# Optimization experiments

Measured on AMD Instinct MI355X. Metric: run time of the kernel, lower is better.

## Reference

```python
import jax, jax.numpy as jnp
import numpy as np
import math

S = 8192  # sequence length
D = 16    # model dim (8-dim one-hot embedding concatenated with its negation)


def _params():
    emb = np.eye(3, 8, dtype=np.float32)
    # ---- FirstLayer ----
    l1_in_w = np.zeros((48, 16), np.float32); l1_in_w[32, 0] = 1; l1_in_w[33, 1] = 1
    l1_in_b = np.zeros(48, np.float32)
    l1_out_w = np.zeros((16, 16), np.float32)
    l1_out_w[3, 0] = 1; l1_out_w[4, 1] = 1; l1_out_w[11, 0] = -1; l1_out_w[12, 1] = -1
    l1_out_b = np.zeros(16, np.float32)
    l1_w1 = np.zeros((16, 16), np.float32)
    l1_w1[5, 3] = 1; l1_w1[5, 4] = -1; l1_w1[6, 3] = -1; l1_w1[6, 4] = 1
    l1_b1 = np.zeros(16, np.float32)
    l1_w2 = np.zeros((16, 16), np.float32)
    l1_w2[5, 5] = 1; l1_w2[6, 6] = 1; l1_w2[7, 5] = 1; l1_w2[7, 6] = 1
    l1_w2[13, 5] = -1; l1_w2[14, 6] = -1; l1_w2[15, 5] = -1; l1_w2[15, 6] = -1
    l1_b2 = np.zeros(16, np.float32)
    # ---- SecondLayer ----
    l2_in_w = np.zeros((48, 16), np.float32)
    l2_in_b = np.zeros(48, np.float32)
    l2_out_w = np.zeros((16, 16), np.float32)
    l2_out_b = np.zeros(16, np.float32)
    l2_w1 = np.zeros((16, 16), np.float32)
    l2_w1[:8, :8] = np.eye(8); l2_w1[8:, :8] = -np.eye(8)
    l2_b1 = np.zeros(16, np.float32)
    A = np.zeros((16, 16), np.float32)
    A[:8, :8] = -np.eye(8); A[:8, 8:] = np.eye(8)
    A[8:, :8] = np.eye(8);  A[8:, 8:] = -np.eye(8)
    B = np.zeros((16, 16), np.float32)
    B[0, 7] = -1; B[0, 15] = 1; B[1, 7] = 1; B[1, 15] = -1
    l2_w2 = A + B
    l2_b2 = np.array([-1e-8] * 8 + [1e-8] * 8, np.float32)
    # ---- Output layer ----
    eta = 1e-5
    c = -(1.0 / math.sqrt(16.0 / 2.0)) * math.log(2.0 ** eta - 1.0)
    ow = np.zeros((1, 16), np.float32); ow[0, 0] = c
    ob = np.zeros(1, np.float32)
    names = ['emb', 'l1_in_w', 'l1_in_b', 'l1_out_w', 'l1_out_b', 'l1_w1', 'l1_b1', 'l1_w2', 'l1_b2',
             'l2_in_w', 'l2_in_b', 'l2_out_w', 'l2_out_b', 'l2_w1', 'l2_b1', 'l2_w2', 'l2_b2', 'ow', 'ob']
    vals = [emb, l1_in_w, l1_in_b, l1_out_w, l1_out_b, l1_w1, l1_b1, l1_w2, l1_b2,
            l2_in_w, l2_in_b, l2_out_w, l2_out_b, l2_w1, l2_b1, l2_w2, l2_b2, ow, ob]
    return {n: jnp.asarray(v) for n, v in zip(names, vals)}


def setup_inputs() -> dict:
    key = jax.random.key(0)
    w = jax.random.randint(key, (S,), 0, 3)
    inp = {'w': w}
    inp.update(_params())
    return inp


def _layernorm(x):
    # hand-rolled layernorm: (x - mean) / sqrt(E[x^2] - mean^2), no eps, no affine
    mean = jnp.mean(x, axis=-1, keepdims=True)
    var = jnp.mean(x * x, axis=-1, keepdims=True) - mean * mean
    return (x - mean) / jnp.sqrt(var)


def _layer(src, in_w, in_b, out_w, out_b, w1, b1, w2, b2):
    # src: [S, 16]; single-head MHA, dropout=0, relu activation
    qw, kw, vw = jnp.split(in_w, 3, axis=0)
    qb, kb, vb = jnp.split(in_b, 3)
    q = src @ qw.T + qb
    k = src @ kw.T + kb
    v = src @ vw.T + vb
    attn = jax.nn.softmax((q @ k.T) / math.sqrt(float(D)), axis=-1)  # [S, S]
    a = (attn @ v) @ out_w.T + out_b
    h = _layernorm(src + a)
    ff = jax.nn.relu(h @ w1.T + b1) @ w2.T + b2
    return _layernorm(h + ff)


def reference(w, emb, l1_in_w, l1_in_b, l1_out_w, l1_out_b, l1_w1, l1_b1, l1_w2, l1_b2,
              l2_in_w, l2_in_b, l2_out_w, l2_out_b, l2_w1, l2_b1, l2_w2, l2_b2, ow, ob):
    x = emb[w]                                    # [S, 8]
    src = jnp.concatenate([x, -x], axis=-1)       # [S, 16]
    src = _layer(src, l1_in_w, l1_in_b, l1_out_w, l1_out_b, l1_w1, l1_b1, l1_w2, l1_b2)
    src = _layer(src, l2_in_w, l2_in_b, l2_out_w, l2_out_b, l2_w1, l2_b1, l2_w2, l2_b2)
    return src[0] @ ow.T + ob                     # [1]
```

## Files before the change

kernel.cpp:

```cpp
#include <hip/hip_runtime.h>


#define NT 256

struct LayerRegs {
    float4 vw[4], ow[4], w1[4], w2[4];
    float vb, ob_, b1, b2;
};

__device__ __forceinline__ float gsum16(float v) {
    v += __shfl_xor(v, 1, 16);
    v += __shfl_xor(v, 2, 16);
    v += __shfl_xor(v, 4, 16);
    v += __shfl_xor(v, 8, 16);
    return v;
}

__device__ __forceinline__ float lnp(float x) {
    float s  = gsum16(x);
    float s2 = gsum16(x * x);
    float mean = s * 0.0625f;
    float msq  = s2 * 0.0625f;
    return (x - mean) * rsqrtf(msq - mean * mean);
}

__device__ __forceinline__ float matR(const float4* __restrict__ W, float b, float x) {
    float a0 = b, a1 = 0.f;
    #pragma unroll
    for (int kq = 0; kq < 4; ++kq) {
        float4 wv = W[kq];
        a0 += __shfl(x, 4 * kq + 0, 16) * wv.x;
        a1 += __shfl(x, 4 * kq + 1, 16) * wv.y;
        a0 += __shfl(x, 4 * kq + 2, 16) * wv.z;
        a1 += __shfl(x, 4 * kq + 3, 16) * wv.w;
    }
    return a0 + a1;
}

__device__ __forceinline__ float layer_lane(float src, float meansrc,
                                            const LayerRegs& L) {
    float vmean = matR(L.vw, L.vb,  meansrc);
    float a     = matR(L.ow, L.ob_, vmean);
    float h     = lnp(src + a);
    float r     = fmaxf(matR(L.w1, L.b1, h), 0.f);
    float y     = h + matR(L.w2, L.b2, r);
    return lnp(y);
}

#define LOADROW(dst, ptr, row) {                         \
    const float4* _p = (const float4*)(ptr) + (row) * 4; \
    dst[0] = _p[0]; dst[1] = _p[1];                      \
    dst[2] = _p[2]; dst[3] = _p[3]; }

__global__ void __launch_bounds__(NT)
model_kernel(const int* __restrict__ w, int S,
             const float* __restrict__ emb,
             const float* __restrict__ l1_in_w, const float* __restrict__ l1_in_b,
             const float* __restrict__ l1_out_w, const float* __restrict__ l1_out_b,
             const float* __restrict__ l1_w1, const float* __restrict__ l1_b1,
             const float* __restrict__ l1_w2, const float* __restrict__ l1_b2,
             const float* __restrict__ l2_in_w, const float* __restrict__ l2_in_b,
             const float* __restrict__ l2_out_w, const float* __restrict__ l2_out_b,
             const float* __restrict__ l2_w1, const float* __restrict__ l2_b1,
             const float* __restrict__ l2_w2, const float* __restrict__ l2_b2,
             const float* __restrict__ ow, const float* __restrict__ ob,
             float* __restrict__ out)
{
    __shared__ int cnt[2];
    const int tid = threadIdx.x;
    const int j   = tid & 15;
    const int jb  = j & 7;
    const bool w0wave = (tid < 64);
    if (tid < 2) cnt[tid] = 0;

    LayerRegs R1, R2;
    float e0 = 0.f, e1 = 0.f, e2 = 0.f, owj = 0.f, ob0 = 0.f;
    int t0 = 0;
    if (w0wave) {
        t0 = w[0];
        LOADROW(R1.vw, l1_in_w, 32 + j);
        LOADROW(R1.ow, l1_out_w, j);
        LOADROW(R1.w1, l1_w1, j);
        LOADROW(R1.w2, l1_w2, j);
        LOADROW(R2.vw, l2_in_w, 32 + j);
        LOADROW(R2.ow, l2_out_w, j);
        LOADROW(R2.w1, l2_w1, j);
        LOADROW(R2.w2, l2_w2, j);
        R1.vb = l1_in_b[32 + j]; R1.ob_ = l1_out_b[j];
        R1.b1 = l1_b1[j];        R1.b2  = l1_b2[j];
        R2.vb = l2_in_b[32 + j]; R2.ob_ = l2_out_b[j];
        R2.b1 = l2_b1[j];        R2.b2  = l2_b2[j];
        e0 = emb[jb]; e1 = emb[8 + jb]; e2 = emb[16 + jb];
        owj = ow[j];  ob0 = ob[0];
    }
    const float invS = 1.f / (float)S;

    int c0 = 0, c1 = 0;
    if (S == NT * 32) {
        const int4* w4 = (const int4*)w;
        int4 t[8];
        #pragma unroll
        for (int u = 0; u < 8; ++u) t[u] = w4[tid + u * NT];
        #pragma unroll
        for (int u = 0; u < 8; ++u) {
            c0 += (t[u].x == 0) + (t[u].y == 0) + (t[u].z == 0) + (t[u].w == 0);
            c1 += (t[u].x == 1) + (t[u].y == 1) + (t[u].z == 1) + (t[u].w == 1);
        }
    } else {
        for (int i = tid; i < S; i += NT) {
            int t = w[i];
            c0 += (t == 0); c1 += (t == 1);
        }
    }
    #pragma unroll
    for (int off = 32; off; off >>= 1) {
        c0 += __shfl_down(c0, off);
        c1 += __shfl_down(c1, off);
    }
    __syncthreads();
    if ((tid & 63) == 0) {
        atomicAdd(&cnt[0], c0);
        atomicAdd(&cnt[1], c1);
    }
    __syncthreads();
    if (!w0wave) return;

    const float p0 = cnt[0] * invS;
    const float p1 = cnt[1] * invS;
    const float p2 = 1.f - p0 - p1;
    const float sgn = (j < 8) ? 1.f : -1.f;

    const float meansrc = sgn * (p0 * e0 + p1 * e1 + p2 * e2);

    const float r0 = layer_lane(sgn * e0, meansrc, R1);
    const float r1 = layer_lane(sgn * e1, meansrc, R1);
    const float r2 = layer_lane(sgn * e2, meansrc, R1);

    const float meansrc1 = p0 * r0 + p1 * r1 + p2 * r2;
    const float src2 = (t0 == 0) ? r0 : (t0 == 1 ? r1 : r2);
    const float fin = layer_lane(src2, meansrc1, R2);

    const float dot = gsum16(fin * owj);
    if (tid == 0) out[0] = dot + ob0;
}

extern "C" void kernel_launch(void* const* d_in, const int* in_sizes, int n_in,
                              void* d_out, int out_size, void* d_ws, size_t ws_size,
                              hipStream_t stream) {
    const int*   w        = (const int*)  d_in[0];
    const int    S        = in_sizes[0];
    const float* emb      = (const float*)d_in[1];
    const float* l1_in_w  = (const float*)d_in[2];
    const float* l1_in_b  = (const float*)d_in[3];
    const float* l1_out_w = (const float*)d_in[4];
    const float* l1_out_b = (const float*)d_in[5];
    const float* l1_w1    = (const float*)d_in[6];
    const float* l1_b1    = (const float*)d_in[7];
    const float* l1_w2    = (const float*)d_in[8];
    const float* l1_b2    = (const float*)d_in[9];
    const float* l2_in_w  = (const float*)d_in[10];
    const float* l2_in_b  = (const float*)d_in[11];
    const float* l2_out_w = (const float*)d_in[12];
    const float* l2_out_b = (const float*)d_in[13];
    const float* l2_w1    = (const float*)d_in[14];
    const float* l2_b1    = (const float*)d_in[15];
    const float* l2_w2    = (const float*)d_in[16];
    const float* l2_b2    = (const float*)d_in[17];
    const float* ow       = (const float*)d_in[18];
    const float* ob       = (const float*)d_in[19];
    float* out = (float*)d_out;

    model_kernel<<<1, NT, 0, stream>>>(w, S, emb,
        l1_in_w, l1_in_b, l1_out_w, l1_out_b, l1_w1, l1_b1, l1_w2, l1_b2,
        l2_in_w, l2_in_b, l2_out_w, l2_out_b, l2_w1, l2_b1, l2_w2, l2_b2,
        ow, ob, out);
}
```

Baseline: 9.930 us.

## Overlap token counting with layer-1 precompute and use ds_swizzle broadcasts

Wave 0 no longer counts tokens. It precomputes the attention output per embedding linearly (u and cvec) while waves 1-3 count tokens with packed 16-bit counters and write per-wave partials to shared memory, removing the atomics and one barrier. The three per-token layer-1 evaluations run in parallel across the four 16-lane groups instead of serially, with cross-lane shuffles gathering results. The 16-lane shuffles become ds_swizzle with immediate patterns. Packing counts into 16 bits limits each count to 65535, and moving the attention output projection through linearity reorders floating-point sums.

```diff
diff --git a/kernel.cpp b/kernel.cpp
--- a/kernel.cpp
+++ b/kernel.cpp
@@ -3,16 +3,15 @@
 
 #define NT 256
 
-struct LayerRegs {
-    float4 vw[4], ow[4], w1[4], w2[4];
-    float vb, ob_, b1, b2;
-};
+template<int K> __device__ __forceinline__ float bc16(float v) {
+    return __int_as_float(__builtin_amdgcn_ds_swizzle(__float_as_int(v), 0x10 | (K << 5)));
+}
+template<int M> __device__ __forceinline__ float xr16(float v) {
+    return __int_as_float(__builtin_amdgcn_ds_swizzle(__float_as_int(v), 0x1f | (M << 10)));
+}
 
 __device__ __forceinline__ float gsum16(float v) {
-    v += __shfl_xor(v, 1, 16);
-    v += __shfl_xor(v, 2, 16);
-    v += __shfl_xor(v, 4, 16);
-    v += __shfl_xor(v, 8, 16);
+    v += xr16<1>(v); v += xr16<2>(v); v += xr16<4>(v); v += xr16<8>(v);
     return v;
 }
 
@@ -24,27 +23,22 @@
     return (x - mean) * rsqrtf(msq - mean * mean);
 }
 
+struct LayerRegs {
+    float4 vw[4], ow[4], w1[4], w2[4];
+    float vb, ob_, b1, b2;
+};
+
 __device__ __forceinline__ float matR(const float4* __restrict__ W, float b, float x) {
     float a0 = b, a1 = 0.f;
-    #pragma unroll
-    for (int kq = 0; kq < 4; ++kq) {
-        float4 wv = W[kq];
-        a0 += __shfl(x, 4 * kq + 0, 16) * wv.x;
-        a1 += __shfl(x, 4 * kq + 1, 16) * wv.y;
-        a0 += __shfl(x, 4 * kq + 2, 16) * wv.z;
-        a1 += __shfl(x, 4 * kq + 3, 16) * wv.w;
-    }
+    a0 += bc16<0 >(x) * W[0].x;  a1 += bc16<1 >(x) * W[0].y;
+    a0 += bc16<2 >(x) * W[0].z;  a1 += bc16<3 >(x) * W[0].w;
+    a0 += bc16<4 >(x) * W[1].x;  a1 += bc16<5 >(x) * W[1].y;
+    a0 += bc16<6 >(x) * W[1].z;  a1 += bc16<7 >(x) * W[1].w;
+    a0 += bc16<8 >(x) * W[2].x;  a1 += bc16<9 >(x) * W[2].y;
+    a0 += bc16<10>(x) * W[2].z;  a1 += bc16<11>(x) * W[2].w;
+    a0 += bc16<12>(x) * W[3].x;  a1 += bc16<13>(x) * W[3].y;
+    a0 += bc16<14>(x) * W[3].z;  a1 += bc16<15>(x) * W[3].w;
     return a0 + a1;
-}
-
-__device__ __forceinline__ float layer_lane(float src, float meansrc,
-                                            const LayerRegs& L) {
-    float vmean = matR(L.vw, L.vb,  meansrc);
-    float a     = matR(L.ow, L.ob_, vmean);
-    float h     = lnp(src + a);
-    float r     = fmaxf(matR(L.w1, L.b1, h), 0.f);
-    float y     = h + matR(L.w2, L.b2, r);
-    return lnp(y);
 }
 
 #define LOADROW(dst, ptr, row) {                         \
@@ -53,7 +47,7 @@
     dst[2] = _p[2]; dst[3] = _p[3]; }
 
 __global__ void __launch_bounds__(NT)
-model_kernel(const int* __restrict__ w, int S,
+model_kernel(const int* __restrict__ wtok, int S,
              const float* __restrict__ emb,
              const float* __restrict__ l1_in_w, const float* __restrict__ l1_in_b,
              const float* __restrict__ l1_out_w, const float* __restrict__ l1_out_b,
@@ -66,18 +60,19 @@
              const float* __restrict__ ow, const float* __restrict__ ob,
              float* __restrict__ out)
 {
-    __shared__ int cnt[2];
+    __shared__ int part[3];
     const int tid = threadIdx.x;
     const int j   = tid & 15;
     const int jb  = j & 7;
-    const bool w0wave = (tid < 64);
-    if (tid < 2) cnt[tid] = 0;
+    const int grp = (tid >> 4) & 3;
+    const bool w0 = (tid < 64);
+    const float sgn = (j < 8) ? 1.f : -1.f;
 
     LayerRegs R1, R2;
-    float e0 = 0.f, e1 = 0.f, e2 = 0.f, owj = 0.f, ob0 = 0.f;
+    float eg = 0.f, owj = 0.f, ob0 = 0.f;
     int t0 = 0;
-    if (w0wave) {
-        t0 = w[0];
+    if (w0) {
+        t0 = wtok[0];
         LOADROW(R1.vw, l1_in_w, 32 + j);
         LOADROW(R1.ow, l1_out_w, j);
         LOADROW(R1.w1, l1_w1, j);
@@ -90,55 +85,62 @@
         R1.b1 = l1_b1[j];        R1.b2  = l1_b2[j];
         R2.vb = l2_in_b[32 + j]; R2.ob_ = l2_out_b[j];
         R2.b1 = l2_b1[j];        R2.b2  = l2_b2[j];
-        e0 = emb[jb]; e1 = emb[8 + jb]; e2 = emb[16 + jb];
-        owj = ow[j];  ob0 = ob[0];
+        eg  = emb[((grp < 2) ? grp : 2) * 8 + jb];
+        owj = ow[j]; ob0 = ob[0];
     }
     const float invS = 1.f / (float)S;
 
-    int c0 = 0, c1 = 0;
-    if (S == NT * 32) {
-        const int4* w4 = (const int4*)w;
-        int4 t[8];
+    float u = 0.f, cvec = 0.f;
+    if (!w0) {
+        int c1 = 0, c2 = 0;
+        const int idx = tid - 64;
+        const int n4 = S >> 2;
+        const int4* w4 = (const int4*)wtok;
+        for (int i = idx; i < n4; i += 192) {
+            int4 t = w4[i];
+            c1 += (t.x == 1) + (t.y == 1) + (t.z == 1) + (t.w == 1);
+            c2 += (t.x == 2) + (t.y == 2) + (t.z == 2) + (t.w == 2);
+        }
+        for (int i = (n4 << 2) + idx; i < S; i += 192) {
+            int t = wtok[i];
+            c1 += (t == 1); c2 += (t == 2);
+        }
+        int pack = c1 | (c2 << 16);
         #pragma unroll
-        for (int u = 0; u < 8; ++u) t[u] = w4[tid + u * NT];
-        #pragma unroll
-        for (int u = 0; u < 8; ++u) {
-            c0 += (t[u].x == 0) + (t[u].y == 0) + (t[u].z == 0) + (t[u].w == 0);
-            c1 += (t[u].x == 1) + (t[u].y == 1) + (t[u].z == 1) + (t[u].w == 1);
-        }
+        for (int off = 32; off; off >>= 1) pack += __shfl_down(pack, off);
+        if ((tid & 63) == 0) part[(tid >> 6) - 1] = pack;
     } else {
-        for (int i = tid; i < S; i += NT) {
-            int t = w[i];
-            c0 += (t == 0); c1 += (t == 1);
-        }
-    }
-    #pragma unroll
-    for (int off = 32; off; off >>= 1) {
-        c0 += __shfl_down(c0, off);
-        c1 += __shfl_down(c1, off);
+        u    = matR(R1.ow, 0.f, matR(R1.vw, 0.f, sgn * eg));
+        cvec = matR(R1.ow, R1.ob_, R1.vb);
     }
     __syncthreads();
-    if ((tid & 63) == 0) {
-        atomicAdd(&cnt[0], c0);
-        atomicAdd(&cnt[1], c1);
-    }
-    __syncthreads();
-    if (!w0wave) return;
+    if (!w0) return;
 
-    const float p0 = cnt[0] * invS;
-    const float p1 = cnt[1] * invS;
-    const float p2 = 1.f - p0 - p1;
-    const float sgn = (j < 8) ? 1.f : -1.f;
+    const int pk = part[0] + part[1] + part[2];
+    const float p1 = (float)(pk & 0xffff) * invS;
+    const float p2 = (float)(pk >> 16)    * invS;
+    const float p0 = 1.f - p1 - p2;
 
-    const float meansrc = sgn * (p0 * e0 + p1 * e1 + p2 * e2);
+    const float a = cvec + p0 * __shfl(u, j, 64)
+                         + p1 * __shfl(u, j + 16, 64)
+                         + p2 * __shfl(u, j + 32, 64);
 
-    const float r0 = layer_lane(sgn * e0, meansrc, R1);
-    const float r1 = layer_lane(sgn * e1, meansrc, R1);
-    const float r2 = layer_lane(sgn * e2, meansrc, R1);
+    const float h  = lnp(sgn * eg + a);
+    const float rr = fmaxf(matR(R1.w1, R1.b1, h), 0.f);
+    const float y  = h + matR(R1.w2, R1.b2, rr);
+    const float r  = lnp(y);
 
-    const float meansrc1 = p0 * r0 + p1 * r1 + p2 * r2;
-    const float src2 = (t0 == 0) ? r0 : (t0 == 1 ? r1 : r2);
-    const float fin = layer_lane(src2, meansrc1, R2);
+    const float ms1 = p0 * __shfl(r, j, 64)
+                    + p1 * __shfl(r, j + 16, 64)
+                    + p2 * __shfl(r, j + 32, 64);
+    const float src2 = __shfl(r, j + (t0 << 4), 64);
+
+    const float vm2 = matR(R2.vw, R2.vb, ms1);
+    const float a2  = matR(R2.ow, R2.ob_, vm2);
+    const float h2  = lnp(src2 + a2);
+    const float rr2 = fmaxf(matR(R2.w1, R2.b1, h2), 0.f);
+    const float y2  = h2 + matR(R2.w2, R2.b2, rr2);
+    const float fin = lnp(y2);
 
     const float dot = gsum16(fin * owj);
     if (tid == 0) out[0] = dot + ob0;
```

New measurement: 9.755 us. About the same (-1.8%).
